# Kernel optimization log

Measured on AMD Instinct MI355X. Metric: run time of the kernel, lower is better.

## Reference

```python
import jax, jax.numpy as jnp
import numpy as np
import math

LN_EPS = 1e-5

def _ln(x, g, b):
    m = jnp.mean(x, -1, keepdims=True)
    v = jnp.mean((x - m) ** 2, -1, keepdims=True)
    return (x - m) / jnp.sqrt(v + LN_EPS) * g + b

def setup_inputs() -> dict:
    key = jax.random.key(0)
    ks = jax.random.split(key, 16)
    B, N, D, V = 2, 512, 128, 16
    w = lambda k, shape: jax.random.normal(k, shape, jnp.float32) * 0.02
    return {
        "scalar": jax.random.normal(ks[0], (B, N, D), jnp.float32),
        "vector": jax.random.normal(ks[1], (B, N, 3, V), jnp.float32),
        "coords": jax.random.normal(ks[2], (B, N, 3), jnp.float32),
        "w_q": w(ks[3], (D, D)), "b_q": jnp.zeros((D,), jnp.float32),
        "w_k": w(ks[4], (D, D)), "b_k": jnp.zeros((D,), jnp.float32),
        "w_v": w(ks[5], (D, D)), "b_v": jnp.zeros((D,), jnp.float32),
        "w_d1": w(ks[6], (1, D)), "b_d1": jnp.zeros((D,), jnp.float32),
        "w_d2": w(ks[7], (D, D)), "b_d2": jnp.zeros((D,), jnp.float32),
        "w_g": w(ks[8], (D, V)), "b_g": jnp.zeros((V,), jnp.float32),
        "w_o": w(ks[9], (D, D)), "b_o": jnp.zeros((D,), jnp.float32),
        "w_f1": w(ks[10], (D, 2 * D)), "b_f1": jnp.zeros((2 * D,), jnp.float32),
        "w_f2": w(ks[11], (2 * D, D)), "b_f2": jnp.zeros((D,), jnp.float32),
        "w_vo": w(ks[12], (V, V)), "b_vo": jnp.zeros((V,), jnp.float32),
        "g_s": jnp.ones((D,), jnp.float32), "be_s": jnp.zeros((D,), jnp.float32),
        "g_v": jnp.ones((V,), jnp.float32), "be_v": jnp.zeros((V,), jnp.float32),
    }

def reference(scalar, vector, coords, w_q, b_q, w_k, b_k, w_v, b_v,
              w_d1, b_d1, w_d2, b_d2, w_g, b_g, w_o, b_o,
              w_f1, b_f1, w_f2, b_f2, w_vo, b_vo, g_s, be_s, g_v, be_v):
    D = scalar.shape[-1]
    # pairwise geometry: [B,N,N,3], [B,N,N,1]
    rel = coords[:, :, None, :] - coords[:, None, :, :]
    dist = jnp.linalg.norm(rel, axis=-1, keepdims=True)
    direction = rel / jnp.maximum(dist, 1e-6)
    sn = _ln(scalar, g_s, be_s)
    q = sn @ w_q + b_q
    k = sn @ w_k + b_k
    v = sn @ w_v + b_v
    # distance-conditioned bias: [B,N,N,D]
    bias = jax.nn.gelu(dist @ w_d1 + b_d1, approximate=False) @ w_d2 + b_d2
    # q_i . (k_j + bias_ij) / sqrt(D)
    logits = (jnp.einsum('bid,bjd->bij', q, k)
              + jnp.einsum('bid,bijd->bij', q, bias)) / math.sqrt(D)
    attn = jax.nn.softmax(logits, axis=-1)
    # sum_j attn_ij * (v_j + bias_ij)
    upd = jnp.einsum('bij,bjd->bid', attn, v) + jnp.einsum('bij,bijd->bid', attn, bias)
    scalar = scalar + (upd @ w_o + b_o)
    h = _ln(scalar, g_s, be_s)
    scalar = scalar + (jax.nn.gelu(h @ w_f1 + b_f1, approximate=False) @ w_f2 + b_f2)
    gate = jax.nn.sigmoid(scalar @ w_g + b_g)  # [B,N,V]
    # sum_j attn_ij * (vector_j + dir_ij * gate_i) decomposed (same math, no BxNxNx3xV tensor)
    agg = (jnp.einsum('bij,bjcv->bicv', attn, vector)
           + jnp.einsum('bij,bijc->bic', attn, direction)[..., None] * gate[:, :, None, :])
    projected = _ln(agg, g_v, be_v) @ w_vo + b_vo
    return scalar, vector + projected
```

## Files before the change

kernel.cpp:

```cpp
#include <hip/hip_runtime.h>
#include <math.h>

#define D 128
#define F 256
#define V 16
#define NSEQ 512
#define NROW 1024
#define MQ 7

__device__ __forceinline__ float gelu_exact(float x) {
    return 0.5f * x * (1.0f + erff(x * 0.70710678118654752f));
}

__device__ __forceinline__ float waveSum(float v) {
#pragma unroll
    for (int o = 32; o; o >>= 1) v += __shfl_xor(v, o);
    return v;
}
__device__ __forceinline__ float waveMax(float v) {
#pragma unroll
    for (int o = 32; o; o >>= 1) v = fmaxf(v, __shfl_xor(v, o));
    return v;
}

__device__ __forceinline__ void build_A(const float* __restrict__ w_d1,
                                        const float* __restrict__ b_d1,
                                        float* A_s, int t) {
    if (t < D) {
        const float gam[MQ] = {0.f, 0.5f, 0.39894228f, 0.f, -0.06649038f, 0.f,
                               0.0099735570f};
        float w = w_d1[t], b = b_d1[t];
        float wp[MQ], bp[MQ];
        wp[0] = 1.f; bp[0] = 1.f;
#pragma unroll
        for (int i = 1; i < MQ; i++) { wp[i] = wp[i - 1] * w; bp[i] = bp[i - 1] * b; }
        float A[MQ];
#pragma unroll
        for (int m = 0; m < MQ; m++) A[m] = 0.f;
#pragma unroll
        for (int k = 1; k < MQ; k++) {
            float g = gam[k];
            if (g == 0.f) continue;
            float C = 1.f;
            for (int m = 0; m <= k; m++) {
                A[m] = fmaf(g * C, wp[m] * bp[k - m], A[m]);
                C = C * (float)(k - m) / (float)(m + 1);
            }
        }
#pragma unroll
        for (int m = 0; m < MQ; m++) A_s[t * MQ + m] = A[m];
    }
}

__global__ __launch_bounds__(1024) void k1_qkv(
    const float* __restrict__ scalar,
    const float* __restrict__ w_q, const float* __restrict__ b_q,
    const float* __restrict__ w_k, const float* __restrict__ b_k,
    const float* __restrict__ w_v, const float* __restrict__ b_v,
    const float* __restrict__ w_d1, const float* __restrict__ b_d1,
    const float* __restrict__ w_d2,
    const float* __restrict__ g_s, const float* __restrict__ be_s,
    float* __restrict__ qg, float* __restrict__ kTg, float* __restrict__ vg,
    float* __restrict__ Gg)
{
    const int t = threadIdx.x, h = t >> 8, u = t & 255, d = u & 127;
    const int w = t >> 6, ln = t & 63;
    const int r0 = blockIdx.x * 4, r = r0 + h;
    __shared__ float sn_s[4][D];
    __shared__ float k_s[4][D];
    __shared__ float pq[8][4][D], pk[8][4][D], pv[8][4][D];
    __shared__ float redA[16], redB[16];

    float x = scalar[(size_t)r * D + d];
    {
        float s = waveSum(x);
        if (ln == 0) redA[w] = s;
    }
    __syncthreads();
    float mean = (redA[4 * h] + redA[4 * h + 1] + redA[4 * h + 2] + redA[4 * h + 3])
               * (1.0f / 256.0f);
    float dv = x - mean;
    {
        float s = waveSum(dv * dv);
        if (ln == 0) redB[w] = s;
    }
    __syncthreads();
    float var = (redB[4 * h] + redB[4 * h + 1] + redB[4 * h + 2] + redB[4 * h + 3])
              * (1.0f / 256.0f);
    sn_s[h][d] = dv * rsqrtf(var + 1e-5f) * g_s[d] + be_s[d];
    __syncthreads();

    {
        const int eo = t >> 7, l = t & 127, e0 = eo * 16;
        float aq[4] = {0, 0, 0, 0}, ak[4] = {0, 0, 0, 0}, av[4] = {0, 0, 0, 0};
#pragma unroll 4
        for (int e = e0; e < e0 + 16; e++) {
            float wq = w_q[e * D + l], wk = w_k[e * D + l], wv = w_v[e * D + l];
#pragma unroll
            for (int rr = 0; rr < 4; rr++) {
                float s = sn_s[rr][e];
                aq[rr] = fmaf(s, wq, aq[rr]);
                ak[rr] = fmaf(s, wk, ak[rr]);
                av[rr] = fmaf(s, wv, av[rr]);
            }
        }
#pragma unroll
        for (int rr = 0; rr < 4; rr++) {
            pq[eo][rr][l] = aq[rr];
            pk[eo][rr][l] = ak[rr];
            pv[eo][rr][l] = av[rr];
        }
    }
    __syncthreads();

    for (int idx = t; idx < 1536; idx += 1024) {
        const int mat = idx >> 9, h2 = (idx >> 7) & 3, l = idx & 127;
        const float* P = (mat == 0) ? &pq[0][0][0]
                       : (mat == 1) ? &pk[0][0][0] : &pv[0][0][0];
        float acc = 0.f;
#pragma unroll
        for (int eo = 0; eo < 8; eo++) acc += P[(eo * 4 + h2) * D + l];
        if (mat == 0)      qg[(size_t)(r0 + h2) * D + l] = acc + b_q[l];
        else if (mat == 1) k_s[h2][l] = acc + b_k[l];
        else               vg[(size_t)(r0 + h2) * D + l] = acc + b_v[l];
    }
    __syncthreads();

    if (t < 512) kTg[(size_t)(t >> 2) * NROW + r0 + (t & 3)] = k_s[t & 3][t >> 2];

    if (blockIdx.x == 0) {
        float* A_s = &pq[0][0][0];
        build_A(w_d1, b_d1, A_s, t);
        __syncthreads();
        if (t < D * MQ) {
            const int m = t >> 7, l = t & 127;
            float acc = 0.f;
#pragma unroll 4
            for (int e = 0; e < D; e++)
                acc = fmaf(w_d2[e * D + l], A_s[e * MQ + m], acc);
            Gg[l * MQ + m] = acc;
        }
    }
}

__global__ __launch_bounds__(1024) void k23(
    const float* __restrict__ coords, const float* __restrict__ vecin,
    const float* __restrict__ scalar,
    const float* __restrict__ qg, const float* __restrict__ kTg,
    const float* __restrict__ vg, const float* __restrict__ Gg,
    const float* __restrict__ b_d2,
    const float* __restrict__ w_o, const float* __restrict__ b_o,
    const float* __restrict__ w_f1, const float* __restrict__ b_f1,
    const float* __restrict__ w_f2, const float* __restrict__ b_f2,
    const float* __restrict__ w_g, const float* __restrict__ b_g,
    const float* __restrict__ w_vo, const float* __restrict__ b_vo,
    const float* __restrict__ g_s, const float* __restrict__ be_s,
    const float* __restrict__ g_v, const float* __restrict__ be_v,
    float* __restrict__ out_s, float* __restrict__ out_v)
{
    const int t = threadIdx.x, h = t >> 8, u = t & 255;
    const int w = t >> 6, ln = t & 63;
    const int r0 = blockIdx.x * 4, r = r0 + h, b = r0 >> 9;
    __shared__ __align__(16) float q2_s[4][D];
    __shared__ float Gl_s[D * MQ];
    __shared__ float P_s[4][MQ];
    __shared__ __align__(16) float attn_s[4][NSEQ];
    __shared__ float scr[4096];
    __shared__ float avp[16][4][48];
    __shared__ float redA[16], redB[16];
    __shared__ float wredM[16][10];
    __shared__ float S_s[4][MQ], adir_s[4][3];
    __shared__ float upd_s[4][D], s1_s[4][D], h_s[4][D];
    __shared__ float t2_s[4][F];
    __shared__ float avec_s[4][48], gate_s[4][V], gp[8][4][V], lnv_s[4][48];

    if (t < 512) q2_s[t >> 7][t & 127] = qg[(size_t)(r0 + (t >> 7)) * D + (t & 127)];
    for (int idx = t; idx < D * MQ; idx += 1024) Gl_s[idx] = Gg[idx];

    const float cix = coords[(size_t)r * 3 + 0];
    const float ciy = coords[(size_t)r * 3 + 1];
    const float ciz = coords[(size_t)r * 3 + 2];
    const float2* cj2 = (const float2*)(coords + ((size_t)b * NSEQ + 2 * u) * 3);
    float2 ca = cj2[0], cb = cj2[1], cc = cj2[2];
    float rx0 = cix - ca.x, ry0 = ciy - ca.y, rz0 = ciz - cb.x;
    float rx1 = cix - cb.y, ry1 = ciy - cc.x, rz1 = ciz - cc.y;
    float d0 = sqrtf(rx0 * rx0 + ry0 * ry0 + rz0 * rz0);
    float d1 = sqrtf(rx1 * rx1 + ry1 * ry1 + rz1 * rz1);
    __syncthreads();

    {
        const int dd = u & 127;
        float qv = q2_s[h][dd];
        float pa[MQ];
#pragma unroll
        for (int m = 0; m < MQ; m++) pa[m] = qv * Gl_s[dd * MQ + m];
        pa[0] = fmaf(qv, b_d2[dd], pa[0]);
#pragma unroll
        for (int m = 0; m < MQ; m++) {
            float s = waveSum(pa[m]);
            if (ln == 0) wredM[w][m] = s;
        }
    }
    __syncthreads();
    if (t < 4 * MQ) {
        const int hh = t / MQ, m = t % MQ;
        P_s[hh][m] = (wredM[4 * hh][m] + wredM[4 * hh + 1][m]
                    + wredM[4 * hh + 2][m] + wredM[4 * hh + 3][m]) * 0.5f;
    }
    __syncthreads();

    float Pr[MQ];
#pragma unroll
    for (int m = 0; m < MQ; m++) Pr[m] = P_s[h][m];
    float s0 = 0.f, s1v = 0.f;
    {
        const float* kTe = kTg + (size_t)b * NSEQ + 2 * u;
        const float4* q4s = (const float4*)(&q2_s[h][0]);
#pragma unroll 8
        for (int e4 = 0; e4 < 32; e4++) {
            float4 qe = q4s[e4];
            float2 k0 = *(const float2*)(kTe + (size_t)(4 * e4 + 0) * NROW);
            float2 k1 = *(const float2*)(kTe + (size_t)(4 * e4 + 1) * NROW);
            float2 k2 = *(const float2*)(kTe + (size_t)(4 * e4 + 2) * NROW);
            float2 k3 = *(const float2*)(kTe + (size_t)(4 * e4 + 3) * NROW);
            s0 = fmaf(qe.x, k0.x, s0); s1v = fmaf(qe.x, k0.y, s1v);
            s0 = fmaf(qe.y, k1.x, s0); s1v = fmaf(qe.y, k1.y, s1v);
            s0 = fmaf(qe.z, k2.x, s0); s1v = fmaf(qe.z, k2.y, s1v);
            s0 = fmaf(qe.w, k3.x, s0); s1v = fmaf(qe.w, k3.y, s1v);
        }
    }
    const float sc = 0.08838834764831844f;
    float bias0 = Pr[MQ - 1], bias1 = Pr[MQ - 1];
#pragma unroll
    for (int m = MQ - 2; m >= 0; m--) {
        bias0 = fmaf(bias0, d0, Pr[m]);
        bias1 = fmaf(bias1, d1, Pr[m]);
    }
    float l0 = (s0 + bias0) * sc, l1 = (s1v + bias1) * sc;

    {
        float mx = waveMax(fmaxf(l0, l1));
        if (ln == 0) redA[w] = mx;
    }
    __syncthreads();
    float mx = fmaxf(fmaxf(redA[4 * h], redA[4 * h + 1]),
                     fmaxf(redA[4 * h + 2], redA[4 * h + 3]));
    float p0 = __expf(l0 - mx), p1 = __expf(l1 - mx);
    {
        float s = waveSum(p0 + p1);
        if (ln == 0) redB[w] = s;
    }
    __syncthreads();
    float inv = 1.0f / (redB[4 * h] + redB[4 * h + 1]
                      + redB[4 * h + 2] + redB[4 * h + 3]);
    float a0 = p0 * inv, a1 = p1 * inv;
    *(float2*)(&attn_s[h][2 * u]) = make_float2(a0, a1);

    {
        float red[10];
        float w0 = a0, w1 = a1;
#pragma unroll
        for (int m = 0; m < MQ; m++) { red[m] = w0 + w1; w0 *= d0; w1 *= d1; }
        float ia0 = a0 * __builtin_amdgcn_rcpf(fmaxf(d0, 1e-6f));
        float ia1 = a1 * __builtin_amdgcn_rcpf(fmaxf(d1, 1e-6f));
        red[7] = fmaf(ia0, rx0, ia1 * rx1);
        red[8] = fmaf(ia0, ry0, ia1 * ry1);
        red[9] = fmaf(ia0, rz0, ia1 * rz1);
#pragma unroll
        for (int m = 0; m < 10; m++) {
            float s = waveSum(red[m]);
            if (ln == 0) wredM[w][m] = s;
        }
    }
    __syncthreads();
    if (t < 40) {
        const int hh = t / 10, m = t % 10;
        float s = wredM[4 * hh][m] + wredM[4 * hh + 1][m]
                + wredM[4 * hh + 2][m] + wredM[4 * hh + 3][m];
        if (m < MQ) S_s[hh][m] = s;
        else        adir_s[hh][m - MQ] = s;
    }

    {
        const int dd = t & 127, jo = t >> 7, jb = 64 * jo;
        const float* vb = vg + ((size_t)b * NSEQ + jb) * D + dd;
        float c0 = 0.f, c1 = 0.f, c2 = 0.f, c3 = 0.f;
#pragma unroll 4
        for (int jj = 0; jj < 64; jj++) {
            float vv = vb[(size_t)jj * D];
            c0 = fmaf(attn_s[0][jb + jj], vv, c0);
            c1 = fmaf(attn_s[1][jb + jj], vv, c1);
            c2 = fmaf(attn_s[2][jb + jj], vv, c2);
            c3 = fmaf(attn_s[3][jb + jj], vv, c3);
        }
        scr[(jo * 4 + 0) * D + dd] = c0;
        scr[(jo * 4 + 1) * D + dd] = c1;
        scr[(jo * 4 + 2) * D + dd] = c2;
        scr[(jo * 4 + 3) * D + dd] = c3;
    }
    if (ln < 48) {
        const int jb = 32 * w;
        const float* vp = vecin + ((size_t)b * NSEQ + jb) * 48 + ln;
        float c0 = 0.f, c1 = 0.f, c2 = 0.f, c3 = 0.f;
#pragma unroll 4
        for (int jj = 0; jj < 32; jj++) {
            float vv = vp[(size_t)jj * 48];
            c0 = fmaf(attn_s[0][jb + jj], vv, c0);
            c1 = fmaf(attn_s[1][jb + jj], vv, c1);
            c2 = fmaf(attn_s[2][jb + jj], vv, c2);
            c3 = fmaf(attn_s[3][jb + jj], vv, c3);
        }
        avp[w][0][ln] = c0; avp[w][1][ln] = c1;
        avp[w][2][ln] = c2; avp[w][3][ln] = c3;
    }
    __syncthreads();

    if (t < 512) {
        const int hh = t >> 7, l = t & 127;
        float acc = 0.f;
#pragma unroll
        for (int jo = 0; jo < 8; jo++) acc += scr[(jo * 4 + hh) * D + l];
        float a = 0.f;
#pragma unroll
        for (int m = 0; m < MQ; m++) a = fmaf(Gl_s[l * MQ + m], S_s[hh][m], a);
        upd_s[hh][l] = acc + a + b_d2[l];
    } else if (t - 512 < 192) {
        const int idx = t - 512, hh = idx / 48, i2 = idx % 48;
        float s = 0.f;
#pragma unroll
        for (int w2 = 0; w2 < 16; w2++) s += avp[w2][hh][i2];
        avec_s[hh][i2] = s;
    }
    __syncthreads();

    {
        const int eo = t >> 7, l = t & 127, e0 = 16 * eo;
        float c0 = 0.f, c1 = 0.f, c2 = 0.f, c3 = 0.f;
#pragma unroll 4
        for (int e = e0; e < e0 + 16; e++) {
            float wv = w_o[e * D + l];
            c0 = fmaf(upd_s[0][e], wv, c0);
            c1 = fmaf(upd_s[1][e], wv, c1);
            c2 = fmaf(upd_s[2][e], wv, c2);
            c3 = fmaf(upd_s[3][e], wv, c3);
        }
        scr[(eo * 4 + 0) * D + l] = c0;
        scr[(eo * 4 + 1) * D + l] = c1;
        scr[(eo * 4 + 2) * D + l] = c2;
        scr[(eo * 4 + 3) * D + l] = c3;
    }
    __syncthreads();
    float xln = 0.f;
    {
        const int hh = (t >> 7) & 3, l = t & 127;
        if (t < 512) {
            float acc = 0.f;
#pragma unroll
            for (int eo = 0; eo < 8; eo++) acc += scr[(eo * 4 + hh) * D + l];
            xln = scalar[(size_t)(r0 + hh) * D + l] + acc + b_o[l];
            s1_s[hh][l] = xln;
        }
        float s = waveSum(xln);
        if (t < 512 && ln == 0) redA[w] = s;
    }
    __syncthreads();
    float dvv = 0.f;
    if (t < 512) {
        const int hh = (t >> 7) & 3;
        float mean = (redA[2 * hh] + redA[2 * hh + 1]) * (1.0f / 128.0f);
        dvv = xln - mean;
    }
    {
        float s = waveSum(dvv * dvv);
        if (t < 512 && ln == 0) redB[w] = s;
    }
    __syncthreads();
    if (t < 512) {
        const int hh = (t >> 7) & 3, l = t & 127;
        float var = (redB[2 * hh] + redB[2 * hh + 1]) * (1.0f / 128.0f);
        h_s[hh][l] = dvv * rsqrtf(var + 1e-5f) * g_s[l] + be_s[l];
    }
    __syncthreads();

    {
        const int f = t & 255, eq = t >> 8, e0 = 32 * eq;
        float c0 = 0.f, c1 = 0.f, c2 = 0.f, c3 = 0.f;
#pragma unroll 4
        for (int e = e0; e < e0 + 32; e++) {
            float wv = w_f1[e * F + f];
            c0 = fmaf(h_s[0][e], wv, c0);
            c1 = fmaf(h_s[1][e], wv, c1);
            c2 = fmaf(h_s[2][e], wv, c2);
            c3 = fmaf(h_s[3][e], wv, c3);
        }
        scr[(eq * 4 + 0) * F + f] = c0;
        scr[(eq * 4 + 1) * F + f] = c1;
        scr[(eq * 4 + 2) * F + f] = c2;
        scr[(eq * 4 + 3) * F + f] = c3;
    }
    __syncthreads();
    {
        const int hh = t >> 8, f = t & 255;
        t2_s[hh][f] = gelu_exact(scr[(0 * 4 + hh) * F + f] + scr[(1 * 4 + hh) * F + f]
                               + scr[(2 * 4 + hh) * F + f] + scr[(3 * 4 + hh) * F + f]
                               + b_f1[f]);
    }
    __syncthreads();

    {
        const int fo = t >> 7, l = t & 127, f0 = 32 * fo;
        float c0 = 0.f, c1 = 0.f, c2 = 0.f, c3 = 0.f;
#pragma unroll 4
        for (int f = f0; f < f0 + 32; f++) {
            float wv = w_f2[f * D + l];
            c0 = fmaf(t2_s[0][f], wv, c0);
            c1 = fmaf(t2_s[1][f], wv, c1);
            c2 = fmaf(t2_s[2][f], wv, c2);
            c3 = fmaf(t2_s[3][f], wv, c3);
        }
        scr[(fo * 4 + 0) * D + l] = c0;
        scr[(fo * 4 + 1) * D + l] = c1;
        scr[(fo * 4 + 2) * D + l] = c2;
        scr[(fo * 4 + 3) * D + l] = c3;
    }
    __syncthreads();
    if (t < 512) {
        const int hh = t >> 7, l = t & 127;
        float acc = 0.f;
#pragma unroll
        for (int fo = 0; fo < 8; fo++) acc += scr[(fo * 4 + hh) * D + l];
        float v2 = s1_s[hh][l] + acc + b_f2[l];
        out_s[(size_t)(r0 + hh) * D + l] = v2;
        s1_s[hh][l] = v2;
    }
    __syncthreads();

    if (t < 512) {
        const int dq = t >> 6, rr = (t >> 4) & 3, vv = t & 15, d2 = 16 * dq;
        float a = 0.f;
#pragma unroll 4
        for (int dd = d2; dd < d2 + 16; dd++)
            a = fmaf(s1_s[rr][dd], w_g[dd * V + vv], a);
        gp[dq][rr][vv] = a;
    }
    __syncthreads();
    if (t < 64) {
        const int rr = t >> 4, vv = t & 15;
        float a = b_g[vv];
#pragma unroll
        for (int dq = 0; dq < 8; dq++) a += gp[dq][rr][vv];
        gate_s[rr][vv] = 1.0f / (1.0f + __expf(-a));
    }
    __syncthreads();

    if (t < 192) {
        const int rr = t / 48, idx = t % 48, c = idx >> 4, vv = idx & 15;
        float agg = avec_s[rr][idx] + adir_s[rr][c] * gate_s[rr][vv];
        float s = agg;
#pragma unroll
        for (int o = 8; o; o >>= 1) s += __shfl_xor(s, o, 16);
        float mean = s * (1.0f / 16.0f);
        float e = agg - mean;
        float s2 = e * e;
#pragma unroll
        for (int o = 8; o; o >>= 1) s2 += __shfl_xor(s2, o, 16);
        float rstd = rsqrtf(s2 * (1.0f / 16.0f) + 1e-5f);
        lnv_s[rr][idx] = e * rstd * g_v[vv] + be_v[vv];
    }
    __syncthreads();
    if (t < 192) {
        const int rr = t / 48, idx = t % 48, c = idx >> 4, vv = idx & 15;
        const int row = r0 + rr;
        float a = b_vo[vv];
#pragma unroll
        for (int w2 = 0; w2 < V; w2++)
            a = fmaf(lnv_s[rr][c * V + w2], w_vo[w2 * V + vv], a);
        out_v[(size_t)row * 48 + idx] = vecin[(size_t)row * 48 + idx] + a;
    }
}

extern "C" void kernel_launch(void* const* d_in, const int* in_sizes, int n_in,
                              void* d_out, int out_size, void* d_ws, size_t ws_size,
                              hipStream_t stream)
{
    (void)in_sizes; (void)n_in; (void)out_size; (void)ws_size;
    const float* scalar = (const float*)d_in[0];
    const float* vecin  = (const float*)d_in[1];
    const float* coords = (const float*)d_in[2];
    const float* w_q  = (const float*)d_in[3];  const float* b_q  = (const float*)d_in[4];
    const float* w_k  = (const float*)d_in[5];  const float* b_k  = (const float*)d_in[6];
    const float* w_v  = (const float*)d_in[7];  const float* b_v  = (const float*)d_in[8];
    const float* w_d1 = (const float*)d_in[9];  const float* b_d1 = (const float*)d_in[10];
    const float* w_d2 = (const float*)d_in[11]; const float* b_d2 = (const float*)d_in[12];
    const float* w_g  = (const float*)d_in[13]; const float* b_g  = (const float*)d_in[14];
    const float* w_o  = (const float*)d_in[15]; const float* b_o  = (const float*)d_in[16];
    const float* w_f1 = (const float*)d_in[17]; const float* b_f1 = (const float*)d_in[18];
    const float* w_f2 = (const float*)d_in[19]; const float* b_f2 = (const float*)d_in[20];
    const float* w_vo = (const float*)d_in[21]; const float* b_vo = (const float*)d_in[22];
    const float* g_s  = (const float*)d_in[23]; const float* be_s = (const float*)d_in[24];
    const float* g_v  = (const float*)d_in[25]; const float* be_v = (const float*)d_in[26];

    float* ws = (float*)d_ws;
    float* qg  = ws;
    float* kTg = ws + 131072;
    float* vg  = ws + 262144;
    float* Gg  = ws + 393216;

    float* out_s = (float*)d_out;
    float* out_v = out_s + 131072;

    hipLaunchKernelGGL(k1_qkv, dim3(NROW / 4), dim3(1024), 0, stream,
                       scalar, w_q, b_q, w_k, b_k, w_v, b_v, w_d1, b_d1,
                       w_d2, g_s, be_s, qg, kTg, vg, Gg);
    hipLaunchKernelGGL(k23, dim3(NROW / 4), dim3(1024), 0, stream,
                       coords, vecin, scalar, qg, kTg, vg, Gg,
                       b_d2, w_o, b_o, w_f1, b_f1, w_f2, b_f2,
                       w_g, b_g, w_vo, b_vo, g_s, be_s, g_v, be_v,
                       out_s, out_v);
}
```

Before: 162.9 us.

## Process two rows per block with doubled grid and shared-memory union

Both kernels now handle 2 rows per 1024-thread block instead of 4, doubling the grid to 512 blocks to fill more CUs. Shared buffers are consolidated into one reused scratch array with transposed [D][2] layouts for float2 loads, and the QK dot product is split across the e-dimension by thread halves. Launch bounds request 8 waves per EU. The trade-off is that each block re-reads the weight matrices for half as many rows, so weight traffic per row doubles.

Result: faster. 157.5 us (-3.3%).

```diff
diff --git a/kernel.cpp b/kernel.cpp
--- a/kernel.cpp
+++ b/kernel.cpp
@@ -52,7 +52,7 @@
     }
 }
 
-__global__ __launch_bounds__(1024) void k1_qkv(
+__global__ __launch_bounds__(1024, 8) void k1_qkv(
     const float* __restrict__ scalar,
     const float* __restrict__ w_q, const float* __restrict__ b_q,
     const float* __restrict__ w_k, const float* __restrict__ b_k,
@@ -63,87 +63,76 @@
     float* __restrict__ qg, float* __restrict__ kTg, float* __restrict__ vg,
     float* __restrict__ Gg)
 {
-    const int t = threadIdx.x, h = t >> 8, u = t & 255, d = u & 127;
-    const int w = t >> 6, ln = t & 63;
-    const int r0 = blockIdx.x * 4, r = r0 + h;
-    __shared__ float sn_s[4][D];
-    __shared__ float k_s[4][D];
-    __shared__ float pq[8][4][D], pk[8][4][D], pv[8][4][D];
+    const int t = threadIdx.x, l = t & 127, h2 = (t >> 7) & 1;
+    const int wvid = t >> 6, ln = t & 63;
+    const int r0 = blockIdx.x * 2, r = r0 + h2;
+    __shared__ __align__(8) float snT[D][2];
+    __shared__ float k_s[2][D];
+    __shared__ float A_s[D * MQ];
+    __shared__ float P3[3][8][2][D];
     __shared__ float redA[16], redB[16];
 
-    float x = scalar[(size_t)r * D + d];
-    {
-        float s = waveSum(x);
-        if (ln == 0) redA[w] = s;
-    }
-    __syncthreads();
-    float mean = (redA[4 * h] + redA[4 * h + 1] + redA[4 * h + 2] + redA[4 * h + 3])
-               * (1.0f / 256.0f);
+    float x = scalar[(size_t)r * D + l];
+    { float s = waveSum(x); if (ln == 0) redA[wvid] = s; }
+    __syncthreads();
+    float mean = 0.f;
+#pragma unroll
+    for (int dd = 0; dd < 4; dd++) mean += redA[4 * dd + 2 * h2] + redA[4 * dd + 2 * h2 + 1];
+    mean *= (1.0f / 512.0f);
     float dv = x - mean;
-    {
-        float s = waveSum(dv * dv);
-        if (ln == 0) redB[w] = s;
-    }
-    __syncthreads();
-    float var = (redB[4 * h] + redB[4 * h + 1] + redB[4 * h + 2] + redB[4 * h + 3])
-              * (1.0f / 256.0f);
-    sn_s[h][d] = dv * rsqrtf(var + 1e-5f) * g_s[d] + be_s[d];
-    __syncthreads();
-
-    {
-        const int eo = t >> 7, l = t & 127, e0 = eo * 16;
-        float aq[4] = {0, 0, 0, 0}, ak[4] = {0, 0, 0, 0}, av[4] = {0, 0, 0, 0};
+    { float s = waveSum(dv * dv); if (ln == 0) redB[wvid] = s; }
+    __syncthreads();
+    float var = 0.f;
+#pragma unroll
+    for (int dd = 0; dd < 4; dd++) var += redB[4 * dd + 2 * h2] + redB[4 * dd + 2 * h2 + 1];
+    var *= (1.0f / 512.0f);
+    if (t < 256) snT[l][h2] = dv * rsqrtf(var + 1e-5f) * g_s[l] + be_s[l];
+    __syncthreads();
+
+    {
+        const int eo = t >> 7, e0 = eo * 16;
+        float aq0 = 0.f, aq1 = 0.f, ak0 = 0.f, ak1 = 0.f, av0 = 0.f, av1 = 0.f;
 #pragma unroll 4
         for (int e = e0; e < e0 + 16; e++) {
+            float2 s2 = *(const float2*)&snT[e][0];
             float wq = w_q[e * D + l], wk = w_k[e * D + l], wv = w_v[e * D + l];
-#pragma unroll
-            for (int rr = 0; rr < 4; rr++) {
-                float s = sn_s[rr][e];
-                aq[rr] = fmaf(s, wq, aq[rr]);
-                ak[rr] = fmaf(s, wk, ak[rr]);
-                av[rr] = fmaf(s, wv, av[rr]);
-            }
-        }
-#pragma unroll
-        for (int rr = 0; rr < 4; rr++) {
-            pq[eo][rr][l] = aq[rr];
-            pk[eo][rr][l] = ak[rr];
-            pv[eo][rr][l] = av[rr];
-        }
-    }
-    __syncthreads();
-
-    for (int idx = t; idx < 1536; idx += 1024) {
-        const int mat = idx >> 9, h2 = (idx >> 7) & 3, l = idx & 127;
-        const float* P = (mat == 0) ? &pq[0][0][0]
-                       : (mat == 1) ? &pk[0][0][0] : &pv[0][0][0];
+            aq0 = fmaf(s2.x, wq, aq0); aq1 = fmaf(s2.y, wq, aq1);
+            ak0 = fmaf(s2.x, wk, ak0); ak1 = fmaf(s2.y, wk, ak1);
+            av0 = fmaf(s2.x, wv, av0); av1 = fmaf(s2.y, wv, av1);
+        }
+        P3[0][eo][0][l] = aq0; P3[0][eo][1][l] = aq1;
+        P3[1][eo][0][l] = ak0; P3[1][eo][1][l] = ak1;
+        P3[2][eo][0][l] = av0; P3[2][eo][1][l] = av1;
+    }
+    __syncthreads();
+
+    if (t < 768) {
+        const int mat = t >> 8, h3 = (t >> 7) & 1, l2 = t & 127;
         float acc = 0.f;
 #pragma unroll
-        for (int eo = 0; eo < 8; eo++) acc += P[(eo * 4 + h2) * D + l];
-        if (mat == 0)      qg[(size_t)(r0 + h2) * D + l] = acc + b_q[l];
-        else if (mat == 1) k_s[h2][l] = acc + b_k[l];
-        else               vg[(size_t)(r0 + h2) * D + l] = acc + b_v[l];
-    }
-    __syncthreads();
-
-    if (t < 512) kTg[(size_t)(t >> 2) * NROW + r0 + (t & 3)] = k_s[t & 3][t >> 2];
+        for (int eo = 0; eo < 8; eo++) acc += P3[mat][eo][h3][l2];
+        if (mat == 0)      qg[(size_t)(r0 + h3) * D + l2] = acc + b_q[l2];
+        else if (mat == 1) k_s[h3][l2] = acc + b_k[l2];
+        else               vg[(size_t)(r0 + h3) * D + l2] = acc + b_v[l2];
+    }
+    __syncthreads();
+    if (t < 256) kTg[(size_t)(t >> 1) * NROW + r0 + (t & 1)] = k_s[t & 1][t >> 1];
 
     if (blockIdx.x == 0) {
-        float* A_s = &pq[0][0][0];
         build_A(w_d1, b_d1, A_s, t);
         __syncthreads();
         if (t < D * MQ) {
-            const int m = t >> 7, l = t & 127;
+            const int m = t >> 7, l2 = t & 127;
             float acc = 0.f;
 #pragma unroll 4
             for (int e = 0; e < D; e++)
-                acc = fmaf(w_d2[e * D + l], A_s[e * MQ + m], acc);
-            Gg[l * MQ + m] = acc;
-        }
-    }
-}
-
-__global__ __launch_bounds__(1024) void k23(
+                acc = fmaf(w_d2[e * D + l2], A_s[e * MQ + m], acc);
+            Gg[l2 * MQ + m] = acc;
+        }
+    }
+}
+
+__global__ __launch_bounds__(1024, 8) void k23(
     const float* __restrict__ coords, const float* __restrict__ vecin,
     const float* __restrict__ scalar,
     const float* __restrict__ qg, const float* __restrict__ kTg,
@@ -158,125 +147,110 @@
     const float* __restrict__ g_v, const float* __restrict__ be_v,
     float* __restrict__ out_s, float* __restrict__ out_v)
 {
-    const int t = threadIdx.x, h = t >> 8, u = t & 255;
-    const int w = t >> 6, ln = t & 63;
-    const int r0 = blockIdx.x * 4, r = r0 + h, b = r0 >> 9;
-    __shared__ __align__(16) float q2_s[4][D];
-    __shared__ float Gl_s[D * MQ];
-    __shared__ float P_s[4][MQ];
-    __shared__ __align__(16) float attn_s[4][NSEQ];
-    __shared__ float scr[4096];
-    __shared__ float avp[16][4][48];
-    __shared__ float redA[16], redB[16];
-    __shared__ float wredM[16][10];
-    __shared__ float S_s[4][MQ], adir_s[4][3];
-    __shared__ float upd_s[4][D], s1_s[4][D], h_s[4][D];
-    __shared__ float t2_s[4][F];
-    __shared__ float avec_s[4][48], gate_s[4][V], gp[8][4][V], lnv_s[4][48];
-
-    if (t < 512) q2_s[t >> 7][t & 127] = qg[(size_t)(r0 + (t >> 7)) * D + (t & 127)];
-    for (int idx = t; idx < D * MQ; idx += 1024) Gl_s[idx] = Gg[idx];
-
+    const int t = threadIdx.x, wvid = t >> 6, ln = t & 63;
+    const int r0 = blockIdx.x * 2, b = blockIdx.x >> 8;
+    __shared__ __align__(16) float RA[5632];
+    __shared__ __align__(8) float qT[D][2];
+    __shared__ float Gl[D * MQ];
+    __shared__ float P_s[2][MQ];
+    __shared__ __align__(8) float updT[D][2], hT[D][2], s1T[D][2];
+    __shared__ __align__(8) float t2T[F][2];
+    __shared__ float S_s[2][MQ], adir_s[2][3], avec_s[2][48];
+    __shared__ float redA[16], redB[16], wredM[16][10];
+    __shared__ float gate_s[2][V], gp[8][2][V], lnv_s[2][48];
+
+    if (t < 256) qT[t & 127][t >> 7] = qg[(size_t)(r0 + (t >> 7)) * D + (t & 127)];
+    if (t < D * MQ) Gl[t] = Gg[t];
+    __syncthreads();
+
+    {
+        const int dd = t & 127, h2 = (t >> 7) & 1;
+        float qv = qT[dd][h2];
+        float pa[MQ];
+#pragma unroll
+        for (int m = 0; m < MQ; m++) pa[m] = qv * Gl[dd * MQ + m];
+        pa[0] = fmaf(qv, b_d2[dd], pa[0]);
+#pragma unroll
+        for (int m = 0; m < MQ; m++) {
+            float s = waveSum(pa[m]);
+            if (ln == 0) wredM[wvid][m] = s;
+        }
+    }
+    __syncthreads();
+    if (t < 2 * MQ) {
+        const int hh = t / MQ, m = t % MQ;
+        float s = 0.f;
+#pragma unroll
+        for (int dd = 0; dd < 4; dd++)
+            s += wredM[4 * dd + 2 * hh][m] + wredM[4 * dd + 2 * hh + 1][m];
+        P_s[hh][m] = s * 0.25f;
+    }
+
+    {
+        const int jj = t & 511, eh = t >> 9;
+        const float* ke = kTg + (size_t)(64 * eh) * NROW + (size_t)b * NSEQ + jj;
+        float c0 = 0.f, c1 = 0.f;
+#pragma unroll 8
+        for (int e = 0; e < 64; e++) {
+            float kv = ke[(size_t)e * NROW];
+            float2 q2 = *(const float2*)&qT[64 * eh + e][0];
+            c0 = fmaf(q2.x, kv, c0);
+            c1 = fmaf(q2.y, kv, c1);
+        }
+        *(float2*)&RA[2048 + (eh * 512 + jj) * 2] = make_float2(c0, c1);
+    }
+    __syncthreads();
+
+    const int h2 = t >> 9, j = t & 511, r = r0 + h2;
     const float cix = coords[(size_t)r * 3 + 0];
     const float ciy = coords[(size_t)r * 3 + 1];
     const float ciz = coords[(size_t)r * 3 + 2];
-    const float2* cj2 = (const float2*)(coords + ((size_t)b * NSEQ + 2 * u) * 3);
-    float2 ca = cj2[0], cb = cj2[1], cc = cj2[2];
-    float rx0 = cix - ca.x, ry0 = ciy - ca.y, rz0 = ciz - cb.x;
-    float rx1 = cix - cb.y, ry1 = ciy - cc.x, rz1 = ciz - cc.y;
-    float d0 = sqrtf(rx0 * rx0 + ry0 * ry0 + rz0 * rz0);
-    float d1 = sqrtf(rx1 * rx1 + ry1 * ry1 + rz1 * rz1);
-    __syncthreads();
-
-    {
-        const int dd = u & 127;
-        float qv = q2_s[h][dd];
-        float pa[MQ];
-#pragma unroll
-        for (int m = 0; m < MQ; m++) pa[m] = qv * Gl_s[dd * MQ + m];
-        pa[0] = fmaf(qv, b_d2[dd], pa[0]);
-#pragma unroll
-        for (int m = 0; m < MQ; m++) {
-            float s = waveSum(pa[m]);
-            if (ln == 0) wredM[w][m] = s;
-        }
-    }
-    __syncthreads();
-    if (t < 4 * MQ) {
-        const int hh = t / MQ, m = t % MQ;
-        P_s[hh][m] = (wredM[4 * hh][m] + wredM[4 * hh + 1][m]
-                    + wredM[4 * hh + 2][m] + wredM[4 * hh + 3][m]) * 0.5f;
-    }
-    __syncthreads();
-
+    const float* cj = coords + ((size_t)b * NSEQ + j) * 3;
+    float rx = cix - cj[0], ry = ciy - cj[1], rz = ciz - cj[2];
+    float dj = sqrtf(rx * rx + ry * ry + rz * rz);
+    float qk = RA[2048 + j * 2 + h2] + RA[2048 + (512 + j) * 2 + h2];
     float Pr[MQ];
 #pragma unroll
-    for (int m = 0; m < MQ; m++) Pr[m] = P_s[h][m];
-    float s0 = 0.f, s1v = 0.f;
-    {
-        const float* kTe = kTg + (size_t)b * NSEQ + 2 * u;
-        const float4* q4s = (const float4*)(&q2_s[h][0]);
-#pragma unroll 8
-        for (int e4 = 0; e4 < 32; e4++) {
-            float4 qe = q4s[e4];
-            float2 k0 = *(const float2*)(kTe + (size_t)(4 * e4 + 0) * NROW);
-            float2 k1 = *(const float2*)(kTe + (size_t)(4 * e4 + 1) * NROW);
-            float2 k2 = *(const float2*)(kTe + (size_t)(4 * e4 + 2) * NROW);
-            float2 k3 = *(const float2*)(kTe + (size_t)(4 * e4 + 3) * NROW);
-            s0 = fmaf(qe.x, k0.x, s0); s1v = fmaf(qe.x, k0.y, s1v);
-            s0 = fmaf(qe.y, k1.x, s0); s1v = fmaf(qe.y, k1.y, s1v);
-            s0 = fmaf(qe.z, k2.x, s0); s1v = fmaf(qe.z, k2.y, s1v);
-            s0 = fmaf(qe.w, k3.x, s0); s1v = fmaf(qe.w, k3.y, s1v);
-        }
-    }
+    for (int m = 0; m < MQ; m++) Pr[m] = P_s[h2][m];
+    float bias = Pr[MQ - 1];
+#pragma unroll
+    for (int m = MQ - 2; m >= 0; m--) bias = fmaf(bias, dj, Pr[m]);
     const float sc = 0.08838834764831844f;
-    float bias0 = Pr[MQ - 1], bias1 = Pr[MQ - 1];
-#pragma unroll
-    for (int m = MQ - 2; m >= 0; m--) {
-        bias0 = fmaf(bias0, d0, Pr[m]);
-        bias1 = fmaf(bias1, d1, Pr[m]);
-    }
-    float l0 = (s0 + bias0) * sc, l1 = (s1v + bias1) * sc;
-
-    {
-        float mx = waveMax(fmaxf(l0, l1));
-        if (ln == 0) redA[w] = mx;
-    }
-    __syncthreads();
-    float mx = fmaxf(fmaxf(redA[4 * h], redA[4 * h + 1]),
-                     fmaxf(redA[4 * h + 2], redA[4 * h + 3]));
-    float p0 = __expf(l0 - mx), p1 = __expf(l1 - mx);
-    {
-        float s = waveSum(p0 + p1);
-        if (ln == 0) redB[w] = s;
-    }
-    __syncthreads();
-    float inv = 1.0f / (redB[4 * h] + redB[4 * h + 1]
-                      + redB[4 * h + 2] + redB[4 * h + 3]);
-    float a0 = p0 * inv, a1 = p1 * inv;
-    *(float2*)(&attn_s[h][2 * u]) = make_float2(a0, a1);
+    float lg = (qk + bias) * sc;
+
+    { float mx = waveMax(lg); if (ln == 0) redA[wvid] = mx; }
+    __syncthreads();
+    float mx = redA[8 * h2];
+#pragma unroll
+    for (int k = 1; k < 8; k++) mx = fmaxf(mx, redA[8 * h2 + k]);
+    float p = __expf(lg - mx);
+    { float s = waveSum(p); if (ln == 0) redB[wvid] = s; }
+    __syncthreads();
+    float lsum = 0.f;
+#pragma unroll
+    for (int k = 0; k < 8; k++) lsum += redB[8 * h2 + k];
+    float a = p / lsum;
+    RA[j * 2 + h2] = a;
 
     {
         float red[10];
-        float w0 = a0, w1 = a1;
-#pragma unroll
-        for (int m = 0; m < MQ; m++) { red[m] = w0 + w1; w0 *= d0; w1 *= d1; }
-        float ia0 = a0 * __builtin_amdgcn_rcpf(fmaxf(d0, 1e-6f));
-        float ia1 = a1 * __builtin_amdgcn_rcpf(fmaxf(d1, 1e-6f));
-        red[7] = fmaf(ia0, rx0, ia1 * rx1);
-        red[8] = fmaf(ia0, ry0, ia1 * ry1);
-        red[9] = fmaf(ia0, rz0, ia1 * rz1);
+        float w0 = a;
+#pragma unroll
+        for (int m = 0; m < MQ; m++) { red[m] = w0; w0 *= dj; }
+        float ia = a * __builtin_amdgcn_rcpf(fmaxf(dj, 1e-6f));
+        red[7] = ia * rx; red[8] = ia * ry; red[9] = ia * rz;
 #pragma unroll
         for (int m = 0; m < 10; m++) {
             float s = waveSum(red[m]);
-            if (ln == 0) wredM[w][m] = s;
-        }
-    }
-    __syncthreads();
-    if (t < 40) {
+            if (ln == 0) wredM[wvid][m] = s;
+        }
+    }
+    __syncthreads();
+    if (t < 20) {
         const int hh = t / 10, m = t % 10;
-        float s = wredM[4 * hh][m] + wredM[4 * hh + 1][m]
-                + wredM[4 * hh + 2][m] + wredM[4 * hh + 3][m];
+        float s = 0.f;
+#pragma unroll
+        for (int k = 0; k < 8; k++) s += wredM[8 * hh + k][m];
         if (m < MQ) S_s[hh][m] = s;
         else        adir_s[hh][m - MQ] = s;
     }
@@ -284,176 +258,164 @@
     {
         const int dd = t & 127, jo = t >> 7, jb = 64 * jo;
         const float* vb = vg + ((size_t)b * NSEQ + jb) * D + dd;
-        float c0 = 0.f, c1 = 0.f, c2 = 0.f, c3 = 0.f;
-#pragma unroll 4
+        float c0 = 0.f, c1 = 0.f;
+#pragma unroll 8
         for (int jj = 0; jj < 64; jj++) {
+            float2 at = *(const float2*)&RA[(jb + jj) * 2];
             float vv = vb[(size_t)jj * D];
-            c0 = fmaf(attn_s[0][jb + jj], vv, c0);
-            c1 = fmaf(attn_s[1][jb + jj], vv, c1);
-            c2 = fmaf(attn_s[2][jb + jj], vv, c2);
-            c3 = fmaf(attn_s[3][jb + jj], vv, c3);
-        }
-        scr[(jo * 4 + 0) * D + dd] = c0;
-        scr[(jo * 4 + 1) * D + dd] = c1;
-        scr[(jo * 4 + 2) * D + dd] = c2;
-        scr[(jo * 4 + 3) * D + dd] = c3;
+            c0 = fmaf(at.x, vv, c0);
+            c1 = fmaf(at.y, vv, c1);
+        }
+        RA[2048 + (jo * 2 + 0) * 128 + dd] = c0;
+        RA[2048 + (jo * 2 + 1) * 128 + dd] = c1;
     }
     if (ln < 48) {
-        const int jb = 32 * w;
+        const int jb = 32 * wvid;
         const float* vp = vecin + ((size_t)b * NSEQ + jb) * 48 + ln;
-        float c0 = 0.f, c1 = 0.f, c2 = 0.f, c3 = 0.f;
+        float c0 = 0.f, c1 = 0.f;
 #pragma unroll 4
         for (int jj = 0; jj < 32; jj++) {
+            float2 at = *(const float2*)&RA[(jb + jj) * 2];
             float vv = vp[(size_t)jj * 48];
-            c0 = fmaf(attn_s[0][jb + jj], vv, c0);
-            c1 = fmaf(attn_s[1][jb + jj], vv, c1);
-            c2 = fmaf(attn_s[2][jb + jj], vv, c2);
-            c3 = fmaf(attn_s[3][jb + jj], vv, c3);
-        }
-        avp[w][0][ln] = c0; avp[w][1][ln] = c1;
-        avp[w][2][ln] = c2; avp[w][3][ln] = c3;
-    }
-    __syncthreads();
-
-    if (t < 512) {
+            c0 = fmaf(at.x, vv, c0);
+            c1 = fmaf(at.y, vv, c1);
+        }
+        RA[4096 + (wvid * 2 + 0) * 48 + ln] = c0;
+        RA[4096 + (wvid * 2 + 1) * 48 + ln] = c1;
+    }
+    __syncthreads();
+
+    if (t < 256) {
         const int hh = t >> 7, l = t & 127;
         float acc = 0.f;
 #pragma unroll
-        for (int jo = 0; jo < 8; jo++) acc += scr[(jo * 4 + hh) * D + l];
-        float a = 0.f;
-#pragma unroll
-        for (int m = 0; m < MQ; m++) a = fmaf(Gl_s[l * MQ + m], S_s[hh][m], a);
-        upd_s[hh][l] = acc + a + b_d2[l];
-    } else if (t - 512 < 192) {
-        const int idx = t - 512, hh = idx / 48, i2 = idx % 48;
+        for (int jo = 0; jo < 8; jo++) acc += RA[2048 + (jo * 2 + hh) * 128 + l];
+        float aa = 0.f;
+#pragma unroll
+        for (int m = 0; m < MQ; m++) aa = fmaf(Gl[l * MQ + m], S_s[hh][m], aa);
+        updT[l][hh] = acc + aa + b_d2[l];
+    } else if (t - 256 < 96) {
+        const int idx = t - 256, hh = idx / 48, i2 = idx % 48;
         float s = 0.f;
 #pragma unroll
-        for (int w2 = 0; w2 < 16; w2++) s += avp[w2][hh][i2];
+        for (int w2 = 0; w2 < 16; w2++) s += RA[4096 + (w2 * 2 + hh) * 48 + i2];
         avec_s[hh][i2] = s;
     }
     __syncthreads();
 
     {
         const int eo = t >> 7, l = t & 127, e0 = 16 * eo;
-        float c0 = 0.f, c1 = 0.f, c2 = 0.f, c3 = 0.f;
+        float c0 = 0.f, c1 = 0.f;
 #pragma unroll 4
         for (int e = e0; e < e0 + 16; e++) {
+            float2 up = *(const float2*)&updT[e][0];
             float wv = w_o[e * D + l];
-            c0 = fmaf(upd_s[0][e], wv, c0);
-            c1 = fmaf(upd_s[1][e], wv, c1);
-            c2 = fmaf(upd_s[2][e], wv, c2);
-            c3 = fmaf(upd_s[3][e], wv, c3);
-        }
-        scr[(eo * 4 + 0) * D + l] = c0;
-        scr[(eo * 4 + 1) * D + l] = c1;
-        scr[(eo * 4 + 2) * D + l] = c2;
-        scr[(eo * 4 + 3) * D + l] = c3;
+            c0 = fmaf(up.x, wv, c0);
+            c1 = fmaf(up.y, wv, c1);
+        }
+        RA[2048 + (eo * 2 + 0) * 128 + l] = c0;
+        RA[2048 + (eo * 2 + 1) * 128 + l] = c1;
     }
     __syncthreads();
     float xln = 0.f;
     {
-        const int hh = (t >> 7) & 3, l = t & 127;
-        if (t < 512) {
+        const int hh = (t >> 7) & 1, l = t & 127;
+        if (t < 256) {
             float acc = 0.f;
 #pragma unroll
-            for (int eo = 0; eo < 8; eo++) acc += scr[(eo * 4 + hh) * D + l];
+            for (int eo = 0; eo < 8; eo++) acc += RA[2048 + (eo * 2 + hh) * 128 + l];
             xln = scalar[(size_t)(r0 + hh) * D + l] + acc + b_o[l];
-            s1_s[hh][l] = xln;
+            s1T[l][hh] = xln;
         }
         float s = waveSum(xln);
-        if (t < 512 && ln == 0) redA[w] = s;
+        if (t < 256 && ln == 0) redA[wvid] = s;
     }
     __syncthreads();
     float dvv = 0.f;
-    if (t < 512) {
-        const int hh = (t >> 7) & 3;
+    if (t < 256) {
+        const int hh = (t >> 7) & 1;
         float mean = (redA[2 * hh] + redA[2 * hh + 1]) * (1.0f / 128.0f);
         dvv = xln - mean;
     }
     {
         float s = waveSum(dvv * dvv);
-        if (t < 512 && ln == 0) redB[w] = s;
+        if (t < 256 && ln == 0) redB[wvid] = s;
+    }
+    __syncthreads();
+    if (t < 256) {
+        const int hh = (t >> 7) & 1, l = t & 127;
+        float var = (redB[2 * hh] + redB[2 * hh + 1]) * (1.0f / 128.0f);
+        hT[l][hh] = dvv * rsqrtf(var + 1e-5f) * g_s[l] + be_s[l];
+    }
+    __syncthreads();
+
+    {
+        const int f = t & 255, eq = t >> 8, e0 = 32 * eq;
+        float c0 = 0.f, c1 = 0.f;
+#pragma unroll 4
+        for (int e = e0; e < e0 + 32; e++) {
+            float2 hv = *(const float2*)&hT[e][0];
+            float wv = w_f1[e * F + f];
+            c0 = fmaf(hv.x, wv, c0);
+            c1 = fmaf(hv.y, wv, c1);
+        }
+        RA[2048 + (eq * 2 + 0) * 256 + f] = c0;
+        RA[2048 + (eq * 2 + 1) * 256 + f] = c1;
     }
     __syncthreads();
     if (t < 512) {
-        const int hh = (t >> 7) & 3, l = t & 127;
-        float var = (redB[2 * hh] + redB[2 * hh + 1]) * (1.0f / 128.0f);
-        h_s[hh][l] = dvv * rsqrtf(var + 1e-5f) * g_s[l] + be_s[l];
-    }
-    __syncthreads();
-
-    {
-        const int f = t & 255, eq = t >> 8, e0 = 32 * eq;
-        float c0 = 0.f, c1 = 0.f, c2 = 0.f, c3 = 0.f;
-#pragma unroll 4
-        for (int e = e0; e < e0 + 32; e++) {
-            float wv = w_f1[e * F + f];
-            c0 = fmaf(h_s[0][e], wv, c0);
-            c1 = fmaf(h_s[1][e], wv, c1);
-            c2 = fmaf(h_s[2][e], wv, c2);
-            c3 = fmaf(h_s[3][e], wv, c3);
-        }
-        scr[(eq * 4 + 0) * F + f] = c0;
-        scr[(eq * 4 + 1) * F + f] = c1;
-        scr[(eq * 4 + 2) * F + f] = c2;
-        scr[(eq * 4 + 3) * F + f] = c3;
-    }
-    __syncthreads();
-    {
         const int hh = t >> 8, f = t & 255;
-        t2_s[hh][f] = gelu_exact(scr[(0 * 4 + hh) * F + f] + scr[(1 * 4 + hh) * F + f]
-                               + scr[(2 * 4 + hh) * F + f] + scr[(3 * 4 + hh) * F + f]
-                               + b_f1[f]);
+        float acc = 0.f;
+#pragma unroll
+        for (int eq = 0; eq < 4; eq++) acc += RA[2048 + (eq * 2 + hh) * 256 + f];
+        t2T[f][hh] = gelu_exact(acc + b_f1[f]);
     }
     __syncthreads();
 
     {
         const int fo = t >> 7, l = t & 127, f0 = 32 * fo;
-        float c0 = 0.f, c1 = 0.f, c2 = 0.f, c3 = 0.f;
+        float c0 = 0.f, c1 = 0.f;
 #pragma unroll 4
         for (int f = f0; f < f0 + 32; f++) {
+            float2 tv = *(const float2*)&t2T[f][0];
             float wv = w_f2[f * D + l];
-            c0 = fmaf(t2_s[0][f], wv, c0);
-            c1 = fmaf(t2_s[1][f], wv, c1);
-            c2 = fmaf(t2_s[2][f], wv, c2);
-            c3 = fmaf(t2_s[3][f], wv, c3);
-        }
-        scr[(fo * 4 + 0) * D + l] = c0;
-        scr[(fo * 4 + 1) * D + l] = c1;
-        scr[(fo * 4 + 2) * D + l] = c2;
-        scr[(fo * 4 + 3) * D + l] = c3;
-    }
-    __syncthreads();
-    if (t < 512) {
+            c0 = fmaf(tv.x, wv, c0);
+            c1 = fmaf(tv.y, wv, c1);
+        }
+        RA[2048 + (fo * 2 + 0) * 128 + l] = c0;
+        RA[2048 + (fo * 2 + 1) * 128 + l] = c1;
+    }
+    __syncthreads();
+    if (t < 256) {
         const int hh = t >> 7, l = t & 127;
         float acc = 0.f;
 #pragma unroll
-        for (int fo = 0; fo < 8; fo++) acc += scr[(fo * 4 + hh) * D + l];
-        float v2 = s1_s[hh][l] + acc + b_f2[l];
+        for (int fo = 0; fo < 8; fo++) acc += RA[2048 + (fo * 2 + hh) * 128 + l];
+        float v2 = s1T[l][hh] + acc + b_f2[l];
         out_s[(size_t)(r0 + hh) * D + l] = v2;
-        s1_s[hh][l] = v2;
-    }
-    __syncthreads();
-
-    if (t < 512) {
-        const int dq = t >> 6, rr = (t >> 4) & 3, vv = t & 15, d2 = 16 * dq;
-        float a = 0.f;
-#pragma unroll 4
-        for (int dd = d2; dd < d2 + 16; dd++)
-            a = fmaf(s1_s[rr][dd], w_g[dd * V + vv], a);
-        gp[dq][rr][vv] = a;
-    }
-    __syncthreads();
-    if (t < 64) {
+        s1T[l][hh] = v2;
+    }
+    __syncthreads();
+
+    if (t < 256) {
+        const int dq = t >> 5, rr = (t >> 4) & 1, vv = t & 15, d0 = 16 * dq;
+        float aa = 0.f;
+#pragma unroll 4
+        for (int dd = d0; dd < d0 + 16; dd++)
+            aa = fmaf(s1T[dd][rr], w_g[dd * V + vv], aa);
+        gp[dq][rr][vv] = aa;
+    }
+    __syncthreads();
+    if (t < 32) {
         const int rr = t >> 4, vv = t & 15;
-        float a = b_g[vv];
-#pragma unroll
-        for (int dq = 0; dq < 8; dq++) a += gp[dq][rr][vv];
-        gate_s[rr][vv] = 1.0f / (1.0f + __expf(-a));
-    }
-    __syncthreads();
-
-    if (t < 192) {
+        float aa = b_g[vv];
+#pragma unroll
+        for (int dq = 0; dq < 8; dq++) aa += gp[dq][rr][vv];
+        gate_s[rr][vv] = 1.0f / (1.0f + __expf(-aa));
+    }
+    __syncthreads();
+
+    if (t < 96) {
         const int rr = t / 48, idx = t % 48, c = idx >> 4, vv = idx & 15;
         float agg = avec_s[rr][idx] + adir_s[rr][c] * gate_s[rr][vv];
         float s = agg;
@@ -468,14 +430,14 @@
         lnv_s[rr][idx] = e * rstd * g_v[vv] + be_v[vv];
     }
     __syncthreads();
-    if (t < 192) {
+    if (t < 96) {
         const int rr = t / 48, idx = t % 48, c = idx >> 4, vv = idx & 15;
         const int row = r0 + rr;
-        float a = b_vo[vv];
+        float aa = b_vo[vv];
 #pragma unroll
         for (int w2 = 0; w2 < V; w2++)
-            a = fmaf(lnv_s[rr][c * V + w2], w_vo[w2 * V + vv], a);
-        out_v[(size_t)row * 48 + idx] = vecin[(size_t)row * 48 + idx] + a;
+            aa = fmaf(lnv_s[rr][c * V + w2], w_vo[w2 * V + vv], aa);
+        out_v[(size_t)row * 48 + idx] = vecin[(size_t)row * 48 + idx] + aa;
     }
 }
 
@@ -500,7 +462,7 @@
     const float* g_s  = (const float*)d_in[23]; const float* be_s = (const float*)d_in[24];
     const float* g_v  = (const float*)d_in[25]; const float* be_v = (const float*)d_in[26];
 
-    float* ws = (float*)d_ws;
+    float* ws  = (float*)d_ws;
     float* qg  = ws;
     float* kTg = ws + 131072;
     float* vg  = ws + 262144;
@@ -509,10 +471,10 @@
     float* out_s = (float*)d_out;
     float* out_v = out_s + 131072;
 
-    hipLaunchKernelGGL(k1_qkv, dim3(NROW / 4), dim3(1024), 0, stream,
+    hipLaunchKernelGGL(k1_qkv, dim3(NROW / 2), dim3(1024), 0, stream,
                        scalar, w_q, b_q, w_k, b_k, w_v, b_v, w_d1, b_d1,
                        w_d2, g_s, be_s, qg, kTg, vg, Gg);
-    hipLaunchKernelGGL(k23, dim3(NROW / 4), dim3(1024), 0, stream,
+    hipLaunchKernelGGL(k23, dim3(NROW / 2), dim3(1024), 0, stream,
                        coords, vecin, scalar, qg, kTg, vg, Gg,
                        b_d2, w_o, b_o, w_f1, b_f1, w_f2, b_f2,
                        w_g, b_g, w_vo, b_vo, g_s, be_s, g_v, be_v,
```
